# Performance work log

Hardware: AMD Instinct MI355X
Metric: run time of the kernel (lower is better)

The kernel has to match this reference:

```python
import jax, jax.numpy as jnp
import numpy as np


def setup_inputs() -> dict:
    key = jax.random.key(0)
    k1, k2 = jax.random.split(key)
    set1 = jax.random.normal(k1, (16384, 3), dtype=jnp.float32)
    set2 = jax.random.normal(k2, (16384, 3), dtype=jnp.float32)
    return {"set1": set1, "set2": set2}


def reference(set1, set2):
    # Pairwise Euclidean distances: [N, M]
    diff = set1[:, None, :] - set2[None, :, :]
    d = jnp.sqrt(jnp.sum(diff * diff, axis=-1))
    term_1 = jnp.mean(jnp.min(d, axis=1))  # mean over N of min over M
    term_2 = jnp.mean(jnp.min(d, axis=0))  # mean over M of min over N
    # directed=False -> symmetric averaged Hausdorff distance
    return term_1 + term_2
```

## Files before the change

### kernel.cpp

```cpp
#include <hip/hip_runtime.h>
#include <hip/hip_bf16.h>
#include <math.h>


#define NPTS   16384
#define BLK    256
#define P      8
#define CHUNK  128
#define XBLK   (NPTS / (BLK * P))
#define SPLIT  (NPTS / CHUNK)
#define NSLICE 4
#define YSL    (SPLIT / NSLICE)
#define FLTMAX 3.402823466e+38f


__global__ __launch_bounds__(BLK, 4)
void pair_part_kernel(const float* __restrict__ s1, const float* __restrict__ s2,
                      float* __restrict__ part ) {
    __shared__ float4 tile[CHUNK];

    const int tid = threadIdx.x;
    const int x   = blockIdx.x;
    const int y   = blockIdx.y;
    const int dir = blockIdx.z;
    const float* __restrict__ A = dir ? s2 : s1;
    const float* __restrict__ B = dir ? s1 : s2;

    const int obase = x * (BLK * P);
    const int cbase = y * CHUNK;

    if (tid < CHUNK) {
        int g = cbase + tid;
        float bx = B[3 * g], by = B[3 * g + 1], bz = B[3 * g + 2];
        tile[tid] = make_float4(bx, by, bz, fmaf(bx, bx, fmaf(by, by, bz * bz)));
    }
    __syncthreads();

    float m2x[P], m2y[P], m2z[P], sa[P], mn[P];
    #pragma unroll
    for (int p = 0; p < P; ++p) {
        int i = obase + p * BLK + tid;
        float ax = A[3 * i], ay = A[3 * i + 1], az = A[3 * i + 2];
        sa[p]  = fmaf(ax, ax, fmaf(ay, ay, az * az));
        m2x[p] = -(ax + ax); m2y[p] = -(ay + ay); m2z[p] = -(az + az);
        mn[p]  = FLTMAX;
    }

    for (int j = 0; j < CHUNK; j += 4) {
        float4 b0 = tile[j], b1 = tile[j + 1], b2 = tile[j + 2], b3 = tile[j + 3];
        #pragma unroll
        for (int p = 0; p < P; ++p) {
            float t0 = fmaf(m2x[p], b0.x, fmaf(m2y[p], b0.y, fmaf(m2z[p], b0.z, b0.w)));
            float t1 = fmaf(m2x[p], b1.x, fmaf(m2y[p], b1.y, fmaf(m2z[p], b1.z, b1.w)));
            float t2 = fmaf(m2x[p], b2.x, fmaf(m2y[p], b2.y, fmaf(m2z[p], b2.z, b2.w)));
            float t3 = fmaf(m2x[p], b3.x, fmaf(m2y[p], b3.y, fmaf(m2z[p], b3.z, b3.w)));
            float u = fminf(fminf(mn[p], t0), t1);
            mn[p] = fminf(fminf(u, t2), t3);
        }
    }

    float* dst = part + ((size_t)dir * SPLIT + y) * NPTS + obase;
    #pragma unroll
    for (int p = 0; p < P; ++p) {
        dst[p * BLK + tid] = fmaxf(sa[p] + mn[p], 0.0f);
    }
}


__global__ __launch_bounds__(BLK)
void reduce_slice_kernel(const float* __restrict__ part, float* __restrict__ part2) {
    const int tid = threadIdx.x;
    const int i   = blockIdx.x * BLK + tid;
    const int sl  = blockIdx.y;
    const int dir = blockIdx.z;

    const float* rp = part + ((size_t)dir * SPLIT + sl * YSL) * NPTS + i;
    float m = FLTMAX;
    #pragma unroll 8
    for (int y = 0; y < YSL; ++y) m = fminf(m, rp[(size_t)y * NPTS]);

    part2[((size_t)dir * NSLICE + sl) * NPTS + i] = m;
}


__global__ __launch_bounds__(BLK)
void reduce_final_kernel(const float* __restrict__ part2, double* __restrict__ blocksum) {
    const int tid = threadIdx.x;
    const int i = blockIdx.x * BLK + tid;

    float r = FLTMAX, c = FLTMAX;
    #pragma unroll
    for (int sl = 0; sl < NSLICE; ++sl) {
        r = fminf(r, part2[(size_t)sl * NPTS + i]);
        c = fminf(c, part2[((size_t)NSLICE + sl) * NPTS + i]);
    }
    double s = (double)sqrtf(r) + (double)sqrtf(c);
    for (int off = 32; off > 0; off >>= 1) s += __shfl_down(s, off);
    __shared__ double w[4];
    if ((tid & 63) == 0) w[tid >> 6] = s;
    __syncthreads();
    if (tid == 0) blocksum[blockIdx.x] = w[0] + w[1] + w[2] + w[3];
}

__global__ void final_kernel(const double* __restrict__ blocksum, float* __restrict__ out) {
    const int lane = threadIdx.x;
    double s = blocksum[lane];
    for (int off = 32; off > 0; off >>= 1) s += __shfl_down(s, off);
    if (lane == 0) out[0] = (float)(s / (double)NPTS);
}


__global__ __launch_bounds__(BLK)
void fb_init(unsigned int* rowmin, unsigned int* colmin) {
    int i = blockIdx.x * BLK + threadIdx.x;
    if (i < NPTS) { rowmin[i] = 0x7F7FFFFFu; colmin[i] = 0x7F7FFFFFu; }
}

__global__ __launch_bounds__(BLK, 4)
void fb_pair(const float* __restrict__ s1, const float* __restrict__ s2,
             unsigned int* __restrict__ rowmin, unsigned int* __restrict__ colmin) {
    __shared__ float4 tile[CHUNK];
    const int tid = threadIdx.x;
    const int dir = blockIdx.z;
    const float* __restrict__ A = dir ? s2 : s1;
    const float* __restrict__ B = dir ? s1 : s2;
    unsigned int* __restrict__ outmin = dir ? colmin : rowmin;
    const int obase = blockIdx.x * (BLK * P);
    const int cbase = blockIdx.y * CHUNK;

    if (tid < CHUNK) {
        int g = cbase + tid;
        float bx = B[3 * g], by = B[3 * g + 1], bz = B[3 * g + 2];
        tile[tid] = make_float4(bx, by, bz, fmaf(bx, bx, fmaf(by, by, bz * bz)));
    }
    __syncthreads();

    float m2x[P], m2y[P], m2z[P], sa[P], mn[P];
    #pragma unroll
    for (int p = 0; p < P; ++p) {
        int i = obase + p * BLK + tid;
        float ax = A[3 * i], ay = A[3 * i + 1], az = A[3 * i + 2];
        sa[p]  = fmaf(ax, ax, fmaf(ay, ay, az * az));
        m2x[p] = -(ax + ax); m2y[p] = -(ay + ay); m2z[p] = -(az + az);
        mn[p]  = FLTMAX;
    }
    for (int j = 0; j < CHUNK; j += 4) {
        float4 b0 = tile[j], b1 = tile[j + 1], b2 = tile[j + 2], b3 = tile[j + 3];
        #pragma unroll
        for (int p = 0; p < P; ++p) {
            float t0 = fmaf(m2x[p], b0.x, fmaf(m2y[p], b0.y, fmaf(m2z[p], b0.z, b0.w)));
            float t1 = fmaf(m2x[p], b1.x, fmaf(m2y[p], b1.y, fmaf(m2z[p], b1.z, b1.w)));
            float t2 = fmaf(m2x[p], b2.x, fmaf(m2y[p], b2.y, fmaf(m2z[p], b2.z, b2.w)));
            float t3 = fmaf(m2x[p], b3.x, fmaf(m2y[p], b3.y, fmaf(m2z[p], b3.z, b3.w)));
            float u = fminf(fminf(mn[p], t0), t1);
            mn[p] = fminf(fminf(u, t2), t3);
        }
    }
    #pragma unroll
    for (int p = 0; p < P; ++p) {
        float d2 = fmaxf(sa[p] + mn[p], 0.0f);
        atomicMin(&outmin[obase + p * BLK + tid], __float_as_uint(d2));
    }
}

__global__ __launch_bounds__(BLK)
void fb_reduce(const unsigned int* __restrict__ rowmin, const unsigned int* __restrict__ colmin,
               double* __restrict__ blocksum) {
    const int tid = threadIdx.x;
    const int i = blockIdx.x * BLK + tid;
    double s = (double)sqrtf(__uint_as_float(rowmin[i]))
             + (double)sqrtf(__uint_as_float(colmin[i]));
    for (int off = 32; off > 0; off >>= 1) s += __shfl_down(s, off);
    __shared__ double w[4];
    if ((tid & 63) == 0) w[tid >> 6] = s;
    __syncthreads();
    if (tid == 0) blocksum[blockIdx.x] = w[0] + w[1] + w[2] + w[3];
}


extern "C" void kernel_launch(void* const* d_in, const int* in_sizes, int n_in,
                              void* d_out, int out_size, void* d_ws, size_t ws_size,
                              hipStream_t stream) {
    const float* s1 = (const float*)d_in[0];
    const float* s2 = (const float*)d_in[1];
    float* out = (float*)d_out;

    const size_t part_elems  = (size_t)2 * SPLIT * NPTS;
    const size_t part2_elems = (size_t)2 * NSLICE * NPTS;
    const size_t need = (part_elems + part2_elems) * sizeof(float) + 64 * sizeof(double);

    if (ws_size >= need) {
        float* part  = (float*)d_ws;
        float* part2 = part + part_elems;
        double* blocksum = (double*)(part2 + part2_elems);

        dim3 grid(XBLK, SPLIT, 2);
        pair_part_kernel<<<grid, BLK, 0, stream>>>(s1, s2, part);
        reduce_slice_kernel<<<dim3(NPTS / BLK, NSLICE, 2), BLK, 0, stream>>>(part, part2);
        reduce_final_kernel<<<NPTS / BLK, BLK, 0, stream>>>(part2, blocksum);
        final_kernel<<<1, 64, 0, stream>>>(blocksum, out);
    } else {
        unsigned int* rowmin = (unsigned int*)d_ws;
        unsigned int* colmin = rowmin + NPTS;
        double* blocksum = (double*)(colmin + NPTS);

        fb_init<<<NPTS / BLK, BLK, 0, stream>>>(rowmin, colmin);
        dim3 grid(XBLK, SPLIT, 2);
        fb_pair<<<grid, BLK, 0, stream>>>(s1, s2, rowmin, colmin);
        fb_reduce<<<NPTS / BLK, BLK, 0, stream>>>(rowmin, colmin, blocksum);
        final_kernel<<<1, 64, 0, stream>>>(blocksum, out);
    }
}
```

Measured before the change: 109.6 us.

## Use packed f32x2 FMA/min with SoA shared tile and larger chunk

Stores the candidate tile as separate x/y/z/norm arrays in shared memory and computes two distances at once with packed float2 vector arithmetic, aiming for packed FMA and min instructions on MI355X. CHUNK is doubled to 256 so every thread loads one tile point, which halves the grid's y dimension and the size of the partial-minimum buffer. The goal is higher VALU throughput in the inner loop and less partial-buffer traffic. In exchange, each block does more serial work and the grid is coarser, and the compiler might not emit packed min.

```diff
diff --git a/kernel.cpp b/kernel.cpp
--- a/kernel.cpp
+++ b/kernel.cpp
@@ -6,18 +6,23 @@
 #define NPTS   16384
 #define BLK    256
 #define P      8
-#define CHUNK  128
+#define CHUNK  256
 #define XBLK   (NPTS / (BLK * P))
 #define SPLIT  (NPTS / CHUNK)
 #define NSLICE 4
 #define YSL    (SPLIT / NSLICE)
 #define FLTMAX 3.402823466e+38f
 
+typedef float f32x2 __attribute__((ext_vector_type(2)));
+
 
 __global__ __launch_bounds__(BLK, 4)
 void pair_part_kernel(const float* __restrict__ s1, const float* __restrict__ s2,
                       float* __restrict__ part ) {
-    __shared__ float4 tile[CHUNK];
+    __shared__ __align__(16) float bxs[CHUNK];
+    __shared__ __align__(16) float bys[CHUNK];
+    __shared__ __align__(16) float bzs[CHUNK];
+    __shared__ __align__(16) float sbs[CHUNK];
 
     const int tid = threadIdx.x;
     const int x   = blockIdx.x;
@@ -29,7 +34,119 @@
     const int obase = x * (BLK * P);
     const int cbase = y * CHUNK;
 
-    if (tid < CHUNK) {
+    {
+        int g = cbase + tid;
+        float bx = B[3 * g], by = B[3 * g + 1], bz = B[3 * g + 2];
+        bxs[tid] = bx; bys[tid] = by; bzs[tid] = bz;
+        sbs[tid] = fmaf(bx, bx, fmaf(by, by, bz * bz));
+    }
+    __syncthreads();
+
+    f32x2 m2x[P], m2y[P], m2z[P], mn2[P];
+    float sa[P];
+    #pragma unroll
+    for (int p = 0; p < P; ++p) {
+        int i = obase + p * BLK + tid;
+        float ax = A[3 * i], ay = A[3 * i + 1], az = A[3 * i + 2];
+        sa[p]  = fmaf(ax, ax, fmaf(ay, ay, az * az));
+        float nx = -(ax + ax), ny = -(ay + ay), nz = -(az + az);
+        m2x[p] = (f32x2){nx, nx}; m2y[p] = (f32x2){ny, ny}; m2z[p] = (f32x2){nz, nz};
+        mn2[p] = (f32x2){FLTMAX, FLTMAX};
+    }
+
+    for (int j = 0; j < CHUNK; j += 4) {
+        float4 vx = *(const float4*)&bxs[j];
+        float4 vy = *(const float4*)&bys[j];
+        float4 vz = *(const float4*)&bzs[j];
+        float4 vw = *(const float4*)&sbs[j];
+        f32x2 bx01 = {vx.x, vx.y}, bx23 = {vx.z, vx.w};
+        f32x2 by01 = {vy.x, vy.y}, by23 = {vy.z, vy.w};
+        f32x2 bz01 = {vz.x, vz.y}, bz23 = {vz.z, vz.w};
+        f32x2 sb01 = {vw.x, vw.y}, sb23 = {vw.z, vw.w};
+        #pragma unroll
+        for (int p = 0; p < P; ++p) {
+            f32x2 t01 = m2z[p] * bz01 + sb01;
+            t01 = m2y[p] * by01 + t01;
+            t01 = m2x[p] * bx01 + t01;
+            f32x2 t23 = m2z[p] * bz23 + sb23;
+            t23 = m2y[p] * by23 + t23;
+            t23 = m2x[p] * bx23 + t23;
+            mn2[p] = __builtin_elementwise_min(mn2[p],
+                     __builtin_elementwise_min(t01, t23));
+        }
+    }
+
+    float* dst = part + ((size_t)dir * SPLIT + y) * NPTS + obase;
+    #pragma unroll
+    for (int p = 0; p < P; ++p) {
+        float m = fminf(mn2[p].x, mn2[p].y);
+        dst[p * BLK + tid] = fmaxf(sa[p] + m, 0.0f);
+    }
+}
+
+
+__global__ __launch_bounds__(BLK)
+void reduce_slice_kernel(const float* __restrict__ part, float* __restrict__ part2) {
+    const int tid = threadIdx.x;
+    const int i   = blockIdx.x * BLK + tid;
+    const int sl  = blockIdx.y;
+    const int dir = blockIdx.z;
+
+    const float* rp = part + ((size_t)dir * SPLIT + sl * YSL) * NPTS + i;
+    float m = FLTMAX;
+    #pragma unroll 8
+    for (int y = 0; y < YSL; ++y) m = fminf(m, rp[(size_t)y * NPTS]);
+
+    part2[((size_t)dir * NSLICE + sl) * NPTS + i] = m;
+}
+
+
+__global__ __launch_bounds__(BLK)
+void reduce_final_kernel(const float* __restrict__ part2, double* __restrict__ blocksum) {
+    const int tid = threadIdx.x;
+    const int i = blockIdx.x * BLK + tid;
+
+    float r = FLTMAX, c = FLTMAX;
+    #pragma unroll
+    for (int sl = 0; sl < NSLICE; ++sl) {
+        r = fminf(r, part2[(size_t)sl * NPTS + i]);
+        c = fminf(c, part2[((size_t)NSLICE + sl) * NPTS + i]);
+    }
+    double s = (double)sqrtf(r) + (double)sqrtf(c);
+    for (int off = 32; off > 0; off >>= 1) s += __shfl_down(s, off);
+    __shared__ double w[4];
+    if ((tid & 63) == 0) w[tid >> 6] = s;
+    __syncthreads();
+    if (tid == 0) blocksum[blockIdx.x] = w[0] + w[1] + w[2] + w[3];
+}
+
+__global__ void final_kernel(const double* __restrict__ blocksum, float* __restrict__ out) {
+    const int lane = threadIdx.x;
+    double s = blocksum[lane];
+    for (int off = 32; off > 0; off >>= 1) s += __shfl_down(s, off);
+    if (lane == 0) out[0] = (float)(s / (double)NPTS);
+}
+
+
+__global__ __launch_bounds__(BLK)
+void fb_init(unsigned int* rowmin, unsigned int* colmin) {
+    int i = blockIdx.x * BLK + threadIdx.x;
+    if (i < NPTS) { rowmin[i] = 0x7F7FFFFFu; colmin[i] = 0x7F7FFFFFu; }
+}
+
+__global__ __launch_bounds__(BLK, 4)
+void fb_pair(const float* __restrict__ s1, const float* __restrict__ s2,
+             unsigned int* __restrict__ rowmin, unsigned int* __restrict__ colmin) {
+    __shared__ float4 tile[CHUNK];
+    const int tid = threadIdx.x;
+    const int dir = blockIdx.z;
+    const float* __restrict__ A = dir ? s2 : s1;
+    const float* __restrict__ B = dir ? s1 : s2;
+    unsigned int* __restrict__ outmin = dir ? colmin : rowmin;
+    const int obase = blockIdx.x * (BLK * P);
+    const int cbase = blockIdx.y * CHUNK;
+
+    {
         int g = cbase + tid;
         float bx = B[3 * g], by = B[3 * g + 1], bz = B[3 * g + 2];
         tile[tid] = make_float4(bx, by, bz, fmaf(bx, bx, fmaf(by, by, bz * bz)));
@@ -45,7 +162,6 @@
         m2x[p] = -(ax + ax); m2y[p] = -(ay + ay); m2z[p] = -(az + az);
         mn[p]  = FLTMAX;
     }
-
     for (int j = 0; j < CHUNK; j += 4) {
         float4 b0 = tile[j], b1 = tile[j + 1], b2 = tile[j + 2], b3 = tile[j + 3];
         #pragma unroll
@@ -58,104 +174,6 @@
             mn[p] = fminf(fminf(u, t2), t3);
         }
     }
-
-    float* dst = part + ((size_t)dir * SPLIT + y) * NPTS + obase;
-    #pragma unroll
-    for (int p = 0; p < P; ++p) {
-        dst[p * BLK + tid] = fmaxf(sa[p] + mn[p], 0.0f);
-    }
-}
-
-
-__global__ __launch_bounds__(BLK)
-void reduce_slice_kernel(const float* __restrict__ part, float* __restrict__ part2) {
-    const int tid = threadIdx.x;
-    const int i   = blockIdx.x * BLK + tid;
-    const int sl  = blockIdx.y;
-    const int dir = blockIdx.z;
-
-    const float* rp = part + ((size_t)dir * SPLIT + sl * YSL) * NPTS + i;
-    float m = FLTMAX;
-    #pragma unroll 8
-    for (int y = 0; y < YSL; ++y) m = fminf(m, rp[(size_t)y * NPTS]);
-
-    part2[((size_t)dir * NSLICE + sl) * NPTS + i] = m;
-}
-
-
-__global__ __launch_bounds__(BLK)
-void reduce_final_kernel(const float* __restrict__ part2, double* __restrict__ blocksum) {
-    const int tid = threadIdx.x;
-    const int i = blockIdx.x * BLK + tid;
-
-    float r = FLTMAX, c = FLTMAX;
-    #pragma unroll
-    for (int sl = 0; sl < NSLICE; ++sl) {
-        r = fminf(r, part2[(size_t)sl * NPTS + i]);
-        c = fminf(c, part2[((size_t)NSLICE + sl) * NPTS + i]);
-    }
-    double s = (double)sqrtf(r) + (double)sqrtf(c);
-    for (int off = 32; off > 0; off >>= 1) s += __shfl_down(s, off);
-    __shared__ double w[4];
-    if ((tid & 63) == 0) w[tid >> 6] = s;
-    __syncthreads();
-    if (tid == 0) blocksum[blockIdx.x] = w[0] + w[1] + w[2] + w[3];
-}
-
-__global__ void final_kernel(const double* __restrict__ blocksum, float* __restrict__ out) {
-    const int lane = threadIdx.x;
-    double s = blocksum[lane];
-    for (int off = 32; off > 0; off >>= 1) s += __shfl_down(s, off);
-    if (lane == 0) out[0] = (float)(s / (double)NPTS);
-}
-
-
-__global__ __launch_bounds__(BLK)
-void fb_init(unsigned int* rowmin, unsigned int* colmin) {
-    int i = blockIdx.x * BLK + threadIdx.x;
-    if (i < NPTS) { rowmin[i] = 0x7F7FFFFFu; colmin[i] = 0x7F7FFFFFu; }
-}
-
-__global__ __launch_bounds__(BLK, 4)
-void fb_pair(const float* __restrict__ s1, const float* __restrict__ s2,
-             unsigned int* __restrict__ rowmin, unsigned int* __restrict__ colmin) {
-    __shared__ float4 tile[CHUNK];
-    const int tid = threadIdx.x;
-    const int dir = blockIdx.z;
-    const float* __restrict__ A = dir ? s2 : s1;
-    const float* __restrict__ B = dir ? s1 : s2;
-    unsigned int* __restrict__ outmin = dir ? colmin : rowmin;
-    const int obase = blockIdx.x * (BLK * P);
-    const int cbase = blockIdx.y * CHUNK;
-
-    if (tid < CHUNK) {
-        int g = cbase + tid;
-        float bx = B[3 * g], by = B[3 * g + 1], bz = B[3 * g + 2];
-        tile[tid] = make_float4(bx, by, bz, fmaf(bx, bx, fmaf(by, by, bz * bz)));
-    }
-    __syncthreads();
-
-    float m2x[P], m2y[P], m2z[P], sa[P], mn[P];
-    #pragma unroll
-    for (int p = 0; p < P; ++p) {
-        int i = obase + p * BLK + tid;
-        float ax = A[3 * i], ay = A[3 * i + 1], az = A[3 * i + 2];
-        sa[p]  = fmaf(ax, ax, fmaf(ay, ay, az * az));
-        m2x[p] = -(ax + ax); m2y[p] = -(ay + ay); m2z[p] = -(az + az);
-        mn[p]  = FLTMAX;
-    }
-    for (int j = 0; j < CHUNK; j += 4) {
-        float4 b0 = tile[j], b1 = tile[j + 1], b2 = tile[j + 2], b3 = tile[j + 3];
-        #pragma unroll
-        for (int p = 0; p < P; ++p) {
-            float t0 = fmaf(m2x[p], b0.x, fmaf(m2y[p], b0.y, fmaf(m2z[p], b0.z, b0.w)));
-            float t1 = fmaf(m2x[p], b1.x, fmaf(m2y[p], b1.y, fmaf(m2z[p], b1.z, b1.w)));
-            float t2 = fmaf(m2x[p], b2.x, fmaf(m2y[p], b2.y, fmaf(m2z[p], b2.z, b2.w)));
-            float t3 = fmaf(m2x[p], b3.x, fmaf(m2y[p], b3.y, fmaf(m2z[p], b3.z, b3.w)));
-            float u = fminf(fminf(mn[p], t0), t1);
-            mn[p] = fminf(fminf(u, t2), t3);
-        }
-    }
     #pragma unroll
     for (int p = 0; p < P; ++p) {
         float d2 = fmaxf(sa[p] + mn[p], 0.0f);
```

After: 109.7 us. No clear change (+0.1%).

## Compute pairwise distance minima with bf16x3-split MFMA instead of scalar FMA

Applied to the files above, without the earlier changes.

A prep kernel splits each coordinate and squared norm into bf16 hi/lo pairs packed into K=32 rows. The pairwise cross term plus the B norm is then computed as one 16x16x32 bf16 MFMA per tile, with running min in registers and shuffle reductions across lanes. The A norm is added in the final reduction. Block tiles are also resized (128x512), which shrinks the partial buffer. This risks precision loss from bf16 splitting and adds a prep pass.

```diff
diff --git a/kernel.cpp b/kernel.cpp
--- a/kernel.cpp
+++ b/kernel.cpp
@@ -5,51 +5,214 @@
 
 #define NPTS   16384
 #define BLK    256
-#define P      8
-#define CHUNK  128
-#define XBLK   (NPTS / (BLK * P))
-#define SPLIT  (NPTS / CHUNK)
+#define MB     128
+#define NB     512
+#define XB     (NPTS / MB)
+#define SPLIT  (NPTS / NB)
 #define NSLICE 4
 #define YSL    (SPLIT / NSLICE)
 #define FLTMAX 3.402823466e+38f
 
+typedef short bf16x8 __attribute__((ext_vector_type(8)));
+typedef float f32x4  __attribute__((ext_vector_type(4)));
+
+__device__ __forceinline__ unsigned short f2b(float v) {
+    unsigned int u = __float_as_uint(v);
+    return (unsigned short)((u + 0x7FFFu + ((u >> 16) & 1u)) >> 16);
+}
+__device__ __forceinline__ float b2f(unsigned short s) {
+    return __uint_as_float(((unsigned int)s) << 16);
+}
+__device__ __forceinline__ unsigned int swz(unsigned int o) {
+    return o ^ (((o >> 6) & 7u) << 4);
+}
+
+
+__device__ __forceinline__
+void pack_point(float x, float y, float z,
+                unsigned short* __restrict__ Arow, unsigned short* __restrict__ Brow,
+                float* __restrict__ sq) {
+    unsigned short hx = f2b(x), hy = f2b(y), hz = f2b(z);
+    float fhx = b2f(hx), fhy = b2f(hy), fhz = b2f(hz);
+    unsigned short lx = f2b(x - fhx), ly = f2b(y - fhy), lz = f2b(z - fhz);
+    unsigned short nhx = f2b(-2.0f * fhx), nhy = f2b(-2.0f * fhy), nhz = f2b(-2.0f * fhz);
+    unsigned short nlx = f2b(-2.0f * b2f(lx)), nly = f2b(-2.0f * b2f(ly)), nlz = f2b(-2.0f * b2f(lz));
+    float s = fmaf(x, x, fmaf(y, y, z * z));
+    unsigned short sh = f2b(s), sl = f2b(s - b2f(sh));
+    unsigned short one = 0x3F80;
+
+    unsigned short A[14] = {nhx,nhy,nhz, nlx,nly,nlz, nhx,nhy,nhz, nlx,nly,nlz, one,one};
+    unsigned short B[14] = { hx, hy, hz,  hx, hy, hz,  lx, ly, lz,  lx, ly, lz,  sh, sl};
+    #pragma unroll
+    for (int k = 0; k < 14; ++k) { Arow[k] = A[k]; Brow[k] = B[k]; }
+    #pragma unroll
+    for (int k = 14; k < 32; ++k) { Arow[k] = 0; Brow[k] = 0; }
+    *sq = s;
+}
+
+__global__ __launch_bounds__(BLK)
+void prep_kernel(const float* __restrict__ s1, const float* __restrict__ s2,
+                 unsigned short* __restrict__ pA1, unsigned short* __restrict__ pB1,
+                 unsigned short* __restrict__ pA2, unsigned short* __restrict__ pB2,
+                 float* __restrict__ sqa1, float* __restrict__ sqa2) {
+    int i = blockIdx.x * BLK + threadIdx.x;
+    pack_point(s1[3*i], s1[3*i+1], s1[3*i+2], pA1 + (size_t)i*32, pB1 + (size_t)i*32, &sqa1[i]);
+    pack_point(s2[3*i], s2[3*i+1], s2[3*i+2], pA2 + (size_t)i*32, pB2 + (size_t)i*32, &sqa2[i]);
+}
+
 
 __global__ __launch_bounds__(BLK, 4)
-void pair_part_kernel(const float* __restrict__ s1, const float* __restrict__ s2,
+void mfma_pair_kernel(const unsigned short* __restrict__ pA1, const unsigned short* __restrict__ pB1,
+                      const unsigned short* __restrict__ pA2, const unsigned short* __restrict__ pB2,
                       float* __restrict__ part ) {
-    __shared__ float4 tile[CHUNK];
-
+    __shared__ __align__(16) unsigned char ldsA[MB * 64];
+    __shared__ __align__(16) unsigned char ldsB[NB * 64];
+
+    const int tid  = threadIdx.x;
+    const int lane = tid & 63;
+    const int w    = tid >> 6;
+    const int x    = blockIdx.x;
+    const int y    = blockIdx.y;
+    const int dir  = blockIdx.z;
+
+    const uint4* Ag = (const uint4*)(dir ? pA2 : pA1);
+    const uint4* Bg = (const uint4*)(dir ? pB1 : pB2);
+    const int obase = x * MB;
+    const int cbase = y * NB;
+
+    #pragma unroll
+    for (int c = 0; c < 2; ++c) {
+        int idx = c * BLK + tid;
+        *(uint4*)&ldsA[swz(idx * 16)] = Ag[(size_t)obase * 4 + idx];
+    }
+    #pragma unroll
+    for (int c = 0; c < 8; ++c) {
+        int idx = c * BLK + tid;
+        *(uint4*)&ldsB[swz(idx * 16)] = Bg[(size_t)cbase * 4 + idx];
+    }
+    __syncthreads();
+
+    const int kg = lane >> 4;
+    const int r0 = w * 32 + (lane & 15);
+    bf16x8 a0 = *(const bf16x8*)&ldsA[swz((unsigned)(r0       * 64 + kg * 16))];
+    bf16x8 a1 = *(const bf16x8*)&ldsA[swz((unsigned)((r0 + 16) * 64 + kg * 16))];
+
+    f32x4 rm0 = {FLTMAX, FLTMAX, FLTMAX, FLTMAX};
+    f32x4 rm1 = {FLTMAX, FLTMAX, FLTMAX, FLTMAX};
+    const f32x4 z4 = {0.0f, 0.0f, 0.0f, 0.0f};
+
+    #pragma unroll 4
+    for (int u = 0; u < NB / 16; ++u) {
+        const int col = u * 16 + (lane & 15);
+        bf16x8 bf = *(const bf16x8*)&ldsB[swz((unsigned)(col * 64 + kg * 16))];
+        f32x4 c0 = __builtin_amdgcn_mfma_f32_16x16x32_bf16(a0, bf, z4, 0, 0, 0);
+        f32x4 c1 = __builtin_amdgcn_mfma_f32_16x16x32_bf16(a1, bf, z4, 0, 0, 0);
+        rm0.x = fminf(rm0.x, c0.x); rm0.y = fminf(rm0.y, c0.y);
+        rm0.z = fminf(rm0.z, c0.z); rm0.w = fminf(rm0.w, c0.w);
+        rm1.x = fminf(rm1.x, c1.x); rm1.y = fminf(rm1.y, c1.y);
+        rm1.z = fminf(rm1.z, c1.z); rm1.w = fminf(rm1.w, c1.w);
+    }
+
+    float* base = part + ((size_t)dir * SPLIT + y) * NPTS;
+    #pragma unroll
+    for (int t = 0; t < 2; ++t) {
+        f32x4 rm = t ? rm1 : rm0;
+        float v0 = rm.x, v1 = rm.y, v2 = rm.z, v3 = rm.w;
+        #pragma unroll
+        for (int m = 1; m <= 8; m <<= 1) {
+            v0 = fminf(v0, __shfl_xor(v0, m));
+            v1 = fminf(v1, __shfl_xor(v1, m));
+            v2 = fminf(v2, __shfl_xor(v2, m));
+            v3 = fminf(v3, __shfl_xor(v3, m));
+        }
+        if ((lane & 15) == 0) {
+            int row = obase + w * 32 + t * 16 + kg * 4;
+            base[row + 0] = v0; base[row + 1] = v1;
+            base[row + 2] = v2; base[row + 3] = v3;
+        }
+    }
+}
+
+
+__global__ __launch_bounds__(BLK)
+void reduce_slice_kernel(const float* __restrict__ part, float* __restrict__ part2) {
+    const int i   = blockIdx.x * BLK + threadIdx.x;
+    const int sl  = blockIdx.y;
+    const int dir = blockIdx.z;
+    const float* rp = part + ((size_t)dir * SPLIT + sl * YSL) * NPTS + i;
+    float m = FLTMAX;
+    #pragma unroll
+    for (int yy = 0; yy < YSL; ++yy) m = fminf(m, rp[(size_t)yy * NPTS]);
+    part2[((size_t)dir * NSLICE + sl) * NPTS + i] = m;
+}
+
+__global__ __launch_bounds__(BLK)
+void reduce_final_kernel(const float* __restrict__ part2,
+                         const float* __restrict__ sqa1, const float* __restrict__ sqa2,
+                         double* __restrict__ blocksum) {
     const int tid = threadIdx.x;
-    const int x   = blockIdx.x;
-    const int y   = blockIdx.y;
+    const int i = blockIdx.x * BLK + tid;
+    float r = FLTMAX, c = FLTMAX;
+    #pragma unroll
+    for (int sl = 0; sl < NSLICE; ++sl) {
+        r = fminf(r, part2[(size_t)sl * NPTS + i]);
+        c = fminf(c, part2[((size_t)NSLICE + sl) * NPTS + i]);
+    }
+    double s = (double)sqrtf(fmaxf(sqa1[i] + r, 0.0f))
+             + (double)sqrtf(fmaxf(sqa2[i] + c, 0.0f));
+    for (int off = 32; off > 0; off >>= 1) s += __shfl_down(s, off);
+    __shared__ double wv[4];
+    if ((tid & 63) == 0) wv[tid >> 6] = s;
+    __syncthreads();
+    if (tid == 0) blocksum[blockIdx.x] = wv[0] + wv[1] + wv[2] + wv[3];
+}
+
+__global__ void final_kernel(const double* __restrict__ blocksum, float* __restrict__ out) {
+    const int lane = threadIdx.x;
+    double s = blocksum[lane];
+    for (int off = 32; off > 0; off >>= 1) s += __shfl_down(s, off);
+    if (lane == 0) out[0] = (float)(s / (double)NPTS);
+}
+
+
+__global__ __launch_bounds__(BLK)
+void fb_init(unsigned int* rowmin, unsigned int* colmin) {
+    int i = blockIdx.x * BLK + threadIdx.x;
+    if (i < NPTS) { rowmin[i] = 0x7F7FFFFFu; colmin[i] = 0x7F7FFFFFu; }
+}
+
+#define FB_P 8
+#define FB_CHUNK 256
+__global__ __launch_bounds__(BLK, 4)
+void fb_pair(const float* __restrict__ s1, const float* __restrict__ s2,
+             unsigned int* __restrict__ rowmin, unsigned int* __restrict__ colmin) {
+    __shared__ float4 tile[FB_CHUNK];
+    const int tid = threadIdx.x;
     const int dir = blockIdx.z;
     const float* __restrict__ A = dir ? s2 : s1;
     const float* __restrict__ B = dir ? s1 : s2;
-
-    const int obase = x * (BLK * P);
-    const int cbase = y * CHUNK;
-
-    if (tid < CHUNK) {
+    unsigned int* __restrict__ outmin = dir ? colmin : rowmin;
+    const int obase = blockIdx.x * (BLK * FB_P);
+    const int cbase = blockIdx.y * FB_CHUNK;
+    {
         int g = cbase + tid;
-        float bx = B[3 * g], by = B[3 * g + 1], bz = B[3 * g + 2];
+        float bx = B[3*g], by = B[3*g+1], bz = B[3*g+2];
         tile[tid] = make_float4(bx, by, bz, fmaf(bx, bx, fmaf(by, by, bz * bz)));
     }
     __syncthreads();
-
-    float m2x[P], m2y[P], m2z[P], sa[P], mn[P];
-    #pragma unroll
-    for (int p = 0; p < P; ++p) {
+    float m2x[FB_P], m2y[FB_P], m2z[FB_P], sa[FB_P], mn[FB_P];
+    #pragma unroll
+    for (int p = 0; p < FB_P; ++p) {
         int i = obase + p * BLK + tid;
-        float ax = A[3 * i], ay = A[3 * i + 1], az = A[3 * i + 2];
-        sa[p]  = fmaf(ax, ax, fmaf(ay, ay, az * az));
-        m2x[p] = -(ax + ax); m2y[p] = -(ay + ay); m2z[p] = -(az + az);
-        mn[p]  = FLTMAX;
-    }
-
-    for (int j = 0; j < CHUNK; j += 4) {
-        float4 b0 = tile[j], b1 = tile[j + 1], b2 = tile[j + 2], b3 = tile[j + 3];
+        float ax = A[3*i], ay = A[3*i+1], az = A[3*i+2];
+        sa[p] = fmaf(ax, ax, fmaf(ay, ay, az * az));
+        m2x[p] = -(ax+ax); m2y[p] = -(ay+ay); m2z[p] = -(az+az);
+        mn[p] = FLTMAX;
+    }
+    for (int j = 0; j < FB_CHUNK; j += 4) {
+        float4 b0 = tile[j], b1 = tile[j+1], b2 = tile[j+2], b3 = tile[j+3];
         #pragma unroll
-        for (int p = 0; p < P; ++p) {
+        for (int p = 0; p < FB_P; ++p) {
             float t0 = fmaf(m2x[p], b0.x, fmaf(m2y[p], b0.y, fmaf(m2z[p], b0.z, b0.w)));
             float t1 = fmaf(m2x[p], b1.x, fmaf(m2y[p], b1.y, fmaf(m2z[p], b1.z, b1.w)));
             float t2 = fmaf(m2x[p], b2.x, fmaf(m2y[p], b2.y, fmaf(m2z[p], b2.z, b2.w)));
@@ -58,109 +221,9 @@
             mn[p] = fminf(fminf(u, t2), t3);
         }
     }
-
-    float* dst = part + ((size_t)dir * SPLIT + y) * NPTS + obase;
-    #pragma unroll
-    for (int p = 0; p < P; ++p) {
-        dst[p * BLK + tid] = fmaxf(sa[p] + mn[p], 0.0f);
-    }
-}
-
-
-__global__ __launch_bounds__(BLK)
-void reduce_slice_kernel(const float* __restrict__ part, float* __restrict__ part2) {
-    const int tid = threadIdx.x;
-    const int i   = blockIdx.x * BLK + tid;
-    const int sl  = blockIdx.y;
-    const int dir = blockIdx.z;
-
-    const float* rp = part + ((size_t)dir * SPLIT + sl * YSL) * NPTS + i;
-    float m = FLTMAX;
-    #pragma unroll 8
-    for (int y = 0; y < YSL; ++y) m = fminf(m, rp[(size_t)y * NPTS]);
-
-    part2[((size_t)dir * NSLICE + sl) * NPTS + i] = m;
-}
-
-
-__global__ __launch_bounds__(BLK)
-void reduce_final_kernel(const float* __restrict__ part2, double* __restrict__ blocksum) {
-    const int tid = threadIdx.x;
-    const int i = blockIdx.x * BLK + tid;
-
-    float r = FLTMAX, c = FLTMAX;
-    #pragma unroll
-    for (int sl = 0; sl < NSLICE; ++sl) {
-        r = fminf(r, part2[(size_t)sl * NPTS + i]);
-        c = fminf(c, part2[((size_t)NSLICE + sl) * NPTS + i]);
-    }
-    double s = (double)sqrtf(r) + (double)sqrtf(c);
-    for (int off = 32; off > 0; off >>= 1) s += __shfl_down(s, off);
-    __shared__ double w[4];
-    if ((tid & 63) == 0) w[tid >> 6] = s;
-    __syncthreads();
-    if (tid == 0) blocksum[blockIdx.x] = w[0] + w[1] + w[2] + w[3];
-}
-
-__global__ void final_kernel(const double* __restrict__ blocksum, float* __restrict__ out) {
-    const int lane = threadIdx.x;
-    double s = blocksum[lane];
-    for (int off = 32; off > 0; off >>= 1) s += __shfl_down(s, off);
-    if (lane == 0) out[0] = (float)(s / (double)NPTS);
-}
-
-
-__global__ __launch_bounds__(BLK)
-void fb_init(unsigned int* rowmin, unsigned int* colmin) {
-    int i = blockIdx.x * BLK + threadIdx.x;
-    if (i < NPTS) { rowmin[i] = 0x7F7FFFFFu; colmin[i] = 0x7F7FFFFFu; }
-}
-
-__global__ __launch_bounds__(BLK, 4)
-void fb_pair(const float* __restrict__ s1, const float* __restrict__ s2,
-             unsigned int* __restrict__ rowmin, unsigned int* __restrict__ colmin) {
-    __shared__ float4 tile[CHUNK];
-    const int tid = threadIdx.x;
-    const int dir = blockIdx.z;
-    const float* __restrict__ A = dir ? s2 : s1;
-    const float* __restrict__ B = dir ? s1 : s2;
-    unsigned int* __restrict__ outmin = dir ? colmin : rowmin;
-    const int obase = blockIdx.x * (BLK * P);
-    const int cbase = blockIdx.y * CHUNK;
-
-    if (tid < CHUNK) {
-        int g = cbase + tid;
-        float bx = B[3 * g], by = B[3 * g + 1], bz = B[3 * g + 2];
-        tile[tid] = make_float4(bx, by, bz, fmaf(bx, bx, fmaf(by, by, bz * bz)));
-    }
-    __syncthreads();
-
-    float m2x[P], m2y[P], m2z[P], sa[P], mn[P];
-    #pragma unroll
-    for (int p = 0; p < P; ++p) {
-        int i = obase + p * BLK + tid;
-        float ax = A[3 * i], ay = A[3 * i + 1], az = A[3 * i + 2];
-        sa[p]  = fmaf(ax, ax, fmaf(ay, ay, az * az));
-        m2x[p] = -(ax + ax); m2y[p] = -(ay + ay); m2z[p] = -(az + az);
-        mn[p]  = FLTMAX;
-    }
-    for (int j = 0; j < CHUNK; j += 4) {
-        float4 b0 = tile[j], b1 = tile[j + 1], b2 = tile[j + 2], b3 = tile[j + 3];
-        #pragma unroll
-        for (int p = 0; p < P; ++p) {
-            float t0 = fmaf(m2x[p], b0.x, fmaf(m2y[p], b0.y, fmaf(m2z[p], b0.z, b0.w)));
-            float t1 = fmaf(m2x[p], b1.x, fmaf(m2y[p], b1.y, fmaf(m2z[p], b1.z, b1.w)));
-            float t2 = fmaf(m2x[p], b2.x, fmaf(m2y[p], b2.y, fmaf(m2z[p], b2.z, b2.w)));
-            float t3 = fmaf(m2x[p], b3.x, fmaf(m2y[p], b3.y, fmaf(m2z[p], b3.z, b3.w)));
-            float u = fminf(fminf(mn[p], t0), t1);
-            mn[p] = fminf(fminf(u, t2), t3);
-        }
-    }
-    #pragma unroll
-    for (int p = 0; p < P; ++p) {
-        float d2 = fmaxf(sa[p] + mn[p], 0.0f);
-        atomicMin(&outmin[obase + p * BLK + tid], __float_as_uint(d2));
-    }
+    #pragma unroll
+    for (int p = 0; p < FB_P; ++p)
+        atomicMin(&outmin[obase + p * BLK + tid], __float_as_uint(fmaxf(sa[p] + mn[p], 0.0f)));
 }
 
 __global__ __launch_bounds__(BLK)
@@ -171,10 +234,10 @@
     double s = (double)sqrtf(__uint_as_float(rowmin[i]))
              + (double)sqrtf(__uint_as_float(colmin[i]));
     for (int off = 32; off > 0; off >>= 1) s += __shfl_down(s, off);
-    __shared__ double w[4];
-    if ((tid & 63) == 0) w[tid >> 6] = s;
-    __syncthreads();
-    if (tid == 0) blocksum[blockIdx.x] = w[0] + w[1] + w[2] + w[3];
+    __shared__ double wv[4];
+    if ((tid & 63) == 0) wv[tid >> 6] = s;
+    __syncthreads();
+    if (tid == 0) blocksum[blockIdx.x] = wv[0] + wv[1] + wv[2] + wv[3];
 }
 
 
@@ -185,29 +248,33 @@
     const float* s2 = (const float*)d_in[1];
     float* out = (float*)d_out;
 
-    const size_t part_elems  = (size_t)2 * SPLIT * NPTS;
-    const size_t part2_elems = (size_t)2 * NSLICE * NPTS;
-    const size_t need = (part_elems + part2_elems) * sizeof(float) + 64 * sizeof(double);
+    char* base = (char*)d_ws;
+    unsigned short* pA1 = (unsigned short*)base;
+    unsigned short* pB1 = pA1 + (size_t)NPTS * 32;
+    unsigned short* pA2 = pB1 + (size_t)NPTS * 32;
+    unsigned short* pB2 = pA2 + (size_t)NPTS * 32;
+    float* sqa1 = (float*)(pB2 + (size_t)NPTS * 32);
+    float* sqa2 = sqa1 + NPTS;
+    float* part  = sqa2 + NPTS;
+    float* part2 = part + (size_t)2 * SPLIT * NPTS;
+    double* blocksum = (double*)(part2 + (size_t)2 * NSLICE * NPTS);
+    const size_t need = (size_t)(blocksum + 64) - (size_t)base + 64;
 
     if (ws_size >= need) {
-        float* part  = (float*)d_ws;
-        float* part2 = part + part_elems;
-        double* blocksum = (double*)(part2 + part2_elems);
-
-        dim3 grid(XBLK, SPLIT, 2);
-        pair_part_kernel<<<grid, BLK, 0, stream>>>(s1, s2, part);
+        prep_kernel<<<NPTS / BLK, BLK, 0, stream>>>(s1, s2, pA1, pB1, pA2, pB2, sqa1, sqa2);
+        dim3 grid(XB, SPLIT, 2);
+        mfma_pair_kernel<<<grid, BLK, 0, stream>>>(pA1, pB1, pA2, pB2, part);
         reduce_slice_kernel<<<dim3(NPTS / BLK, NSLICE, 2), BLK, 0, stream>>>(part, part2);
-        reduce_final_kernel<<<NPTS / BLK, BLK, 0, stream>>>(part2, blocksum);
+        reduce_final_kernel<<<NPTS / BLK, BLK, 0, stream>>>(part2, sqa1, sqa2, blocksum);
         final_kernel<<<1, 64, 0, stream>>>(blocksum, out);
     } else {
         unsigned int* rowmin = (unsigned int*)d_ws;
         unsigned int* colmin = rowmin + NPTS;
-        double* blocksum = (double*)(colmin + NPTS);
-
+        double* bsum = (double*)(colmin + NPTS);
         fb_init<<<NPTS / BLK, BLK, 0, stream>>>(rowmin, colmin);
-        dim3 grid(XBLK, SPLIT, 2);
+        dim3 grid(NPTS / (BLK * FB_P), NPTS / FB_CHUNK, 2);
         fb_pair<<<grid, BLK, 0, stream>>>(s1, s2, rowmin, colmin);
-        fb_reduce<<<NPTS / BLK, BLK, 0, stream>>>(rowmin, colmin, blocksum);
-        final_kernel<<<1, 64, 0, stream>>>(blocksum, out);
-    }
-}
+        fb_reduce<<<NPTS / BLK, BLK, 0, stream>>>(rowmin, colmin, bsum);
+        final_kernel<<<1, 64, 0, stream>>>(bsum, out);
+    }
+}
```

Result: faster. 102.0 us (-6.9%).
